# Kernel tuning notes

Measured on AMD Instinct MI355X. Metric: run time of the kernel, lower is better.

Reference implementation:

```python
import jax, jax.numpy as jnp
import numpy as np

CURV_BOUNDS = (-2.0, 2.0)
THRESH = 0.01   # |k| below this -> Euclidean branch
EPS = 1e-5

B, S, D = 4, 2048, 512


def setup_inputs() -> dict:
    key = jax.random.key(0)
    ks = jax.random.split(key, 8)
    x = jax.random.normal(ks[0], (B, S, D), jnp.float32)
    sc = 1.0 / np.sqrt(D)  # ~ nn.Linear default init scale
    Wq = jax.random.uniform(ks[1], (D, D), jnp.float32, -sc, sc)
    bq = jax.random.uniform(ks[2], (D,), jnp.float32, -sc, sc)
    Wk = jax.random.uniform(ks[3], (D, D), jnp.float32, -sc, sc)
    bk = jax.random.uniform(ks[4], (D,), jnp.float32, -sc, sc)
    Wv = jax.random.uniform(ks[5], (D, D), jnp.float32, -sc, sc)
    bv = jax.random.uniform(ks[6], (D,), jnp.float32, -sc, sc)
    curvature_raw = jnp.float32(0.5)   # init_curvature
    temperature = jnp.float32(1.0)
    mask = jnp.triu(jnp.ones((S, S), dtype=bool), 1)  # causal: True = masked out
    return {"x": x, "Wq": Wq, "bq": bq, "Wk": Wk, "bk": bk, "Wv": Wv,
            "bv": bv, "curvature_raw": curvature_raw,
            "temperature": temperature, "mask": mask}


def _curvature(raw):
    k_min, k_max = CURV_BOUNDS
    return k_min + (k_max - k_min) * (jnp.tanh(raw) + 1.0) / 2.0


def _project(u, k):
    # project_to_manifold: identity (euclid), Poincare-ball clip (k<0), sphere renorm (k>0)
    n = jnp.sqrt(jnp.sum(u * u, axis=-1, keepdims=True) + 1e-12)
    absk = jnp.abs(k)
    sk = jnp.sqrt(jnp.maximum(absk, EPS))
    max_norm = (1.0 - 1e-3) / sk                      # ball radius 1/sqrt(|k|)
    u_hyp = u * jnp.minimum(1.0, max_norm / n)
    u_sph = u / (n * sk)                              # sphere radius 1/sqrt(k)
    return jnp.where(absk < THRESH, u, jnp.where(k < 0, u_hyp, u_sph))


def reference(x, Wq, bq, Wk, bk, Wv, bv, curvature_raw, temperature, mask):
    k = _curvature(curvature_raw)
    q = x @ Wq.T + bq
    kk = x @ Wk.T + bk
    v = x @ Wv.T + bv
    qm = _project(q, k)
    km = _project(kk, k)

    # pairwise quantities without materializing [B,S,S,D]
    dots = jnp.einsum('bid,bjd->bij', qm, km)         # [B,S,S]
    qn2 = jnp.sum(qm * qm, axis=-1)                   # [B,S]
    kn2 = jnp.sum(km * km, axis=-1)                   # [B,S]
    diff2 = jnp.maximum(qn2[:, :, None] + kn2[:, None, :] - 2.0 * dots, 0.0)

    absk = jnp.abs(k)
    sk = jnp.sqrt(jnp.maximum(absk, EPS))

    d_euc = jnp.sqrt(diff2 + 1e-12)
    # hyperbolic (Poincare ball, c=|k|): acosh(1 + 2c|x-y|^2 / ((1-c|x|^2)(1-c|y|^2))) / sqrt(c)
    denom = jnp.maximum((1.0 - absk * qn2)[:, :, None] * (1.0 - absk * kn2)[:, None, :], EPS)
    arg = 1.0 + 2.0 * absk * diff2 / denom
    d_hyp = jnp.arccosh(jnp.maximum(arg, 1.0 + 1e-7)) / sk
    # spherical (radius 1/sqrt(k)): arccos(k * <x,y>) / sqrt(k)
    cosang = jnp.clip(absk * dots, -1.0 + 1e-7, 1.0 - 1e-7)
    d_sph = jnp.arccos(cosang) / sk

    dist = jnp.where(absk < THRESH, d_euc, jnp.where(k < 0, d_hyp, d_sph))

    scores = -dist / (temperature + 1e-8)
    scores = jnp.where(mask[None, :, :], -jnp.inf, scores)
    attention = jax.nn.softmax(scores, axis=-1)       # [B,S,S]
    output = jnp.einsum('bij,bjd->bid', attention, v) # [B,S,D]
    return output, attention
```

## Files before the change

### kernel.cpp

```cpp
#include <hip/hip_runtime.h>
#include <hip/hip_bf16.h>
#include <math.h>

typedef unsigned short u16;
typedef float float4e __attribute__((ext_vector_type(4)));
typedef short short8 __attribute__((ext_vector_type(8)));
typedef unsigned short ushort8 __attribute__((ext_vector_type(8)));
typedef unsigned short u16x4 __attribute__((ext_vector_type(4)));

#define SEQ 2048
#define DIM 512
#define NB  4

__device__ __forceinline__ float bf2f(u16 h) {
    return __uint_as_float(((unsigned)h) << 16);
}
__device__ __forceinline__ u16 f2bf(float f) {
    __hip_bfloat16 h = __float2bfloat16(f);
    return *reinterpret_cast<u16*>(&h);
}
__device__ __forceinline__ float curv_of(float raw) {
    return -2.0f + 2.0f * (tanhf(raw) + 1.0f);
}
__device__ __forceinline__ void gl_lds16(const u16* g, u16* lds) {
    __builtin_amdgcn_global_load_lds(
        (const __attribute__((address_space(1))) unsigned int*)g,
        (__attribute__((address_space(3))) unsigned int*)lds, 16, 0, 0);
}

__global__ __launch_bounds__(256) void cvt_all_kernel(
    const float* __restrict__ x, const float* __restrict__ Wq,
    const float* __restrict__ Wk, const float* __restrict__ Wv,
    u16* __restrict__ x_bf, u16* __restrict__ Wcat, float* __restrict__ lsum,
    float* __restrict__ outz)
{
    const int n_x = NB * SEQ * DIM, n_w = DIM * DIM;
    const int n_out = NB * SEQ * DIM;
    int gid = blockIdx.x * 256 + threadIdx.x;
    if (gid < NB * SEQ) lsum[gid] = 0.f;
    if (gid < n_out / 4) ((float4*)outz)[gid] = (float4){0.f, 0.f, 0.f, 0.f};
    int i4 = gid * 4;
    if (i4 < n_x) {
        float4 v = *(const float4*)&x[i4];
        u16x4 h = {f2bf(v.x), f2bf(v.y), f2bf(v.z), f2bf(v.w)};
        *(u16x4*)&x_bf[i4] = h;
    } else if (i4 < n_x + 3 * n_w) {
        int j = i4 - n_x;
        const float* W = (j < n_w) ? Wq : (j < 2 * n_w ? Wk : Wv);
        int off = j % n_w;
        float4 v = *(const float4*)&W[off];
        u16x4 h = {f2bf(v.x), f2bf(v.y), f2bf(v.z), f2bf(v.w)};
        *(u16x4*)&Wcat[j] = h;
    }
}

template<int MODE>
__global__ __launch_bounds__(256, 2) void gemm128_kernel(
    const u16* __restrict__ A, int lda, long long sA,
    const u16* __restrict__ Bt, int ldb, long long sB,
    void* __restrict__ Cv, int ldc, long long sC,
    u16* __restrict__ vT,
    float* __restrict__ lsum,
    const float* __restrict__ bq, const float* __restrict__ bk, const float* __restrict__ bv,
    const float* __restrict__ qn2v, const float* __restrict__ kn2v,
    const float* __restrict__ curvp, const float* __restrict__ tempp)
{
    int bn = blockIdx.x, bm = blockIdx.y, b = blockIdx.z;
    if (MODE == 1 && bn > bm) return;

    __shared__ __align__(16) u16 As[128 * 64];
    __shared__ __align__(16) u16 Bs[128 * 64];

    int t = threadIdx.x, wave = t >> 6, lane = t & 63;
    int wr = wave >> 1, wc = wave & 1;
    int lrow = lane & 15, quad = lane >> 4;
    int srow = lane >> 3, sc8 = lane & 7;

    const u16* Ab = A + (size_t)b * sA + (size_t)(bm * 128) * lda;
    const u16* Bb = Bt + (size_t)b * sB + (size_t)(bn * 128) * ldb;

    float4e acc[4][4];
#pragma unroll
    for (int i = 0; i < 4; i++)
#pragma unroll
        for (int j = 0; j < 4; j++) acc[i][j] = (float4e){0.f, 0.f, 0.f, 0.f};

    for (int kt = 0; kt < 8; ++kt) {
        int k0 = kt << 6;
        __syncthreads();
#pragma unroll
        for (int h = 0; h < 4; ++h) {
            int q = wave * 4 + h;
            int row = q * 8 + srow;
            int c = sc8 ^ (row & 7);
            gl_lds16(Ab + (size_t)row * lda + k0 + c * 8, &As[q * 512]);
            gl_lds16(Bb + (size_t)row * ldb + k0 + c * 8, &Bs[q * 512]);
        }
        __syncthreads();
#pragma unroll
        for (int kk = 0; kk < 2; ++kk) {
            short8 af[4], bfr[4];
#pragma unroll
            for (int im = 0; im < 4; im++) {
                int R = wr * 64 + im * 16 + lrow;
                af[im] = *(const short8*)&As[R * 64 + (((kk * 4 + quad) ^ (R & 7)) * 8)];
            }
#pragma unroll
            for (int in = 0; in < 4; in++) {
                int R = wc * 64 + in * 16 + lrow;
                bfr[in] = *(const short8*)&Bs[R * 64 + (((kk * 4 + quad) ^ (R & 7)) * 8)];
            }
#pragma unroll
            for (int im = 0; im < 4; im++)
#pragma unroll
                for (int in = 0; in < 4; in++)
                    acc[im][in] = __builtin_amdgcn_mfma_f32_16x16x32_bf16(af[im], bfr[in], acc[im][in], 0, 0, 0);
        }
    }

    if (MODE == 0) {
        u16* Cb = (u16*)Cv;
#pragma unroll
        for (int in = 0; in < 4; in++) {
            int gj = bn * 128 + wc * 64 + in * 16 + lrow;
            float bias = (gj < 512) ? bq[gj] : (gj < 1024 ? bk[gj - 512] : bv[gj - 1024]);
#pragma unroll
            for (int im = 0; im < 4; im++) {
                int gi0 = bm * 128 + wr * 64 + im * 16 + quad * 4;
                u16x4 pack;
#pragma unroll
                for (int r = 0; r < 4; r++) {
                    u16 hv = f2bf(acc[im][in][r] + bias);
                    Cb[(size_t)(gi0 + r) * ldc + gj] = hv;
                    pack[r] = hv;
                }
                if (gj >= 1024) {
                    int bb = gi0 >> 11, s = gi0 & 2047;
                    *(u16x4*)&vT[((size_t)bb * DIM + (gj - 1024)) * SEQ + s] = pack;
                }
            }
        }
    } else {
        float kv = curv_of(curvp[0]);
        float absk = fabsf(kv);
        float sk = sqrtf(fmaxf(absk, 1e-5f));
        float invT = 1.0f / (tempp[0] + 1e-8f);
        float Cexp = -1.4426950408889634f * invT;
        u16* Cb = (u16*)Cv + (size_t)b * sC;

        float psum[4][4];
#pragma unroll
        for (int im = 0; im < 4; im++)
#pragma unroll
            for (int r = 0; r < 4; r++) psum[im][r] = 0.f;

        float kn[4];
#pragma unroll
        for (int in = 0; in < 4; in++)
            kn[in] = kn2v[b * SEQ + bn * 128 + wc * 64 + in * 16 + lrow];

#pragma unroll
        for (int im = 0; im < 4; im++) {
#pragma unroll
            for (int r = 0; r < 4; r++) {
                int gi = bm * 128 + wr * 64 + im * 16 + quad * 4 + r;
                float qn = qn2v[b * SEQ + gi];
#pragma unroll
                for (int in = 0; in < 4; in++) {
                    int gj = bn * 128 + wc * 64 + in * 16 + lrow;
                    float dot = acc[im][in][r];
                    float diff2 = fmaxf(qn + kn[in] - 2.f * dot, 0.f);
                    float dist;
                    if (absk < 0.01f) {
                        dist = sqrtf(diff2 + 1e-12f);
                    } else if (kv < 0.f) {
                        float denom = fmaxf((1.f - absk * qn) * (1.f - absk * kn[in]), 1e-5f);
                        float arg = fmaxf(1.f + 2.f * absk * diff2 / denom, 1.f + 1e-7f);
                        dist = acoshf(arg) / sk;
                    } else {
                        float c = fminf(fmaxf(absk * dot, -1.f + 1e-7f), 1.f - 1e-7f);
                        dist = acosf(c) / sk;
                    }
                    float e = (gj <= gi) ? exp2f(dist * Cexp) : 0.f;
                    Cb[(size_t)gi * ldc + gj] = f2bf(e);
                    psum[im][r] += e;
                }
            }
        }
#pragma unroll
        for (int im = 0; im < 4; im++)
#pragma unroll
            for (int r = 0; r < 4; r++) {
                float v = psum[im][r];
                v += __shfl_xor(v, 1);
                v += __shfl_xor(v, 2);
                v += __shfl_xor(v, 4);
                v += __shfl_xor(v, 8);
                if (lrow == 0) {
                    int gi = bm * 128 + wr * 64 + im * 16 + quad * 4 + r;
                    atomicAdd(&lsum[b * SEQ + gi], v);
                }
            }
    }
}

template<int MODE>
__global__ __launch_bounds__(256, 8) void gemm64_kernel(
    const u16* __restrict__ A, int lda, long long sA,
    const u16* __restrict__ Bt, int ldb, long long sB,
    void* __restrict__ Cv, int ldc, long long sC,
    u16* __restrict__ vT,
    float* __restrict__ lsum,
    const float* __restrict__ bq, const float* __restrict__ bk, const float* __restrict__ bv,
    const float* __restrict__ qn2v, const float* __restrict__ kn2v,
    const float* __restrict__ curvp, const float* __restrict__ tempp)
{
    int bx = blockIdx.x, bm = blockIdx.y, b = blockIdx.z;
    int bn = (MODE == 2) ? (bx & 7) : bx;
    int kp = (MODE == 2) ? (bx >> 3) : 0;
    if (MODE == 1 && bn > bm) return;

    __shared__ __align__(16) u16 As[64 * 64];
    __shared__ __align__(16) u16 Bs[64 * 64];

    int t = threadIdx.x, wave = t >> 6, lane = t & 63;
    int wr = wave >> 1, wc = wave & 1;
    int lrow = lane & 15, quad = lane >> 4;
    int srow = lane >> 3, sc = lane & 7;

    const u16* Ab = A + (size_t)b * sA + (size_t)(bm * 64) * lda;
    const u16* Bb = Bt + (size_t)b * sB + (size_t)(bn * 64) * ldb;

    float4e acc[2][2];
#pragma unroll
    for (int i = 0; i < 2; i++)
#pragma unroll
        for (int j = 0; j < 2; j++) acc[i][j] = (float4e){0.f, 0.f, 0.f, 0.f};

    int ktBeg = (MODE == 2) ? kp : 0;
    int ktEnd = (MODE == 2) ? (bm + 1) : 8;
    int ktStp = (MODE == 2) ? 2 : 1;

    for (int kt = ktBeg; kt < ktEnd; kt += ktStp) {
        int k0 = kt << 6;
        __syncthreads();
#pragma unroll
        for (int h = 0; h < 2; ++h) {
            int q = wave * 2 + h;
            int row = q * 8 + srow;
            int c = sc ^ (row & 7);
            gl_lds16(Ab + (size_t)row * lda + k0 + c * 8, &As[q * 512]);
            gl_lds16(Bb + (size_t)row * ldb + k0 + c * 8, &Bs[q * 512]);
        }
        __syncthreads();
#pragma unroll
        for (int s = 0; s < 2; ++s) {
            short8 af[2], bfr[2];
#pragma unroll
            for (int im = 0; im < 2; im++) {
                int R = wr * 32 + im * 16 + lrow;
                af[im] = *(const short8*)&As[R * 64 + (((s * 4 + quad) ^ (R & 7)) * 8)];
            }
#pragma unroll
            for (int in = 0; in < 2; in++) {
                int R = wc * 32 + in * 16 + lrow;
                bfr[in] = *(const short8*)&Bs[R * 64 + (((s * 4 + quad) ^ (R & 7)) * 8)];
            }
#pragma unroll
            for (int im = 0; im < 2; im++)
#pragma unroll
                for (int in = 0; in < 2; in++)
                    acc[im][in] = __builtin_amdgcn_mfma_f32_16x16x32_bf16(af[im], bfr[in], acc[im][in], 0, 0, 0);
        }
    }

    if (MODE == 2) {
        float* Cb = (float*)Cv + (size_t)b * sC;
#pragma unroll
        for (int im = 0; im < 2; im++)
#pragma unroll
            for (int r = 0; r < 4; r++) {
                int gi = bm * 64 + wr * 32 + im * 16 + quad * 4 + r;
                float invl = 1.0f / lsum[b * SEQ + gi];
#pragma unroll
                for (int in = 0; in < 2; in++) {
                    int gd = bn * 64 + wc * 32 + in * 16 + lrow;
                    atomicAdd(&Cb[(size_t)gi * ldc + gd], acc[im][in][r] * invl);
                }
            }
    }
}

__global__ __launch_bounds__(256) void project_kernel(
    const u16* __restrict__ qkvh,
    u16* __restrict__ qm, u16* __restrict__ km,
    float* __restrict__ qn2, float* __restrict__ kn2,
    const float* __restrict__ curvp)
{
    int wave = threadIdx.x >> 6, lane = threadIdx.x & 63;
    int r = blockIdx.x * 4 + wave;
    float kv = curv_of(curvp[0]);
    float absk = fabsf(kv);
    float sk = sqrtf(fmaxf(absk, 1e-5f));

    const u16* qrow = qkvh + (size_t)r * 1536;
    ushort8 qh = *(const ushort8*)&qrow[lane * 8];
    ushort8 kh = *(const ushort8*)&qrow[512 + lane * 8];

    float qv[8], kw[8];
    float sq = 0.f, s2 = 0.f;
#pragma unroll
    for (int e = 0; e < 8; e++) {
        qv[e] = bf2f(qh[e]); sq += qv[e] * qv[e];
        kw[e] = bf2f(kh[e]); s2 += kw[e] * kw[e];
    }
#pragma unroll
    for (int off = 1; off < 64; off <<= 1) {
        sq += __shfl_xor(sq, off);
        s2 += __shfl_xor(s2, off);
    }

    float sclq, sclk;
    {
        float nq = sqrtf(sq + 1e-12f);
        float nk = sqrtf(s2 + 1e-12f);
        if (absk < 0.01f) { sclq = 1.f; sclk = 1.f; }
        else if (kv < 0.f) {
            float mx = (1.0f - 1e-3f) / sk;
            sclq = fminf(1.f, mx / nq);
            sclk = fminf(1.f, mx / nk);
        } else {
            sclq = 1.f / (nq * sk);
            sclk = 1.f / (nk * sk);
        }
    }
    if (lane == 0) {
        qn2[r] = sq * sclq * sclq;
        kn2[r] = s2 * sclk * sclk;
    }
    ushort8 qo, ko;
#pragma unroll
    for (int e = 0; e < 8; e++) {
        qo[e] = f2bf(qv[e] * sclq);
        ko[e] = f2bf(kw[e] * sclk);
    }
    *(ushort8*)&qm[(size_t)r * 512 + lane * 8] = qo;
    *(ushort8*)&km[(size_t)r * 512 + lane * 8] = ko;
}

__global__ __launch_bounds__(256) void norm_attn_kernel(
    const u16* __restrict__ attnH, const float* __restrict__ lsum,
    float* __restrict__ attnF)
{
    int i = blockIdx.x, b = blockIdx.y, t = threadIdx.x;
    float inv = 1.0f / lsum[b * SEQ + i];
    const u16* rowh = attnH + ((size_t)b * SEQ + i) * SEQ;
    float* row = attnF + ((size_t)b * SEQ + i) * SEQ;
    int L = i + 1;
    int j0 = t * 8;
    float4 lo, hi;
    if (j0 + 8 <= L) {
        ushort8 h = *(const ushort8*)&rowh[j0];
        lo.x = bf2f(h[0]) * inv; lo.y = bf2f(h[1]) * inv;
        lo.z = bf2f(h[2]) * inv; lo.w = bf2f(h[3]) * inv;
        hi.x = bf2f(h[4]) * inv; hi.y = bf2f(h[5]) * inv;
        hi.z = bf2f(h[6]) * inv; hi.w = bf2f(h[7]) * inv;
    } else {
        float v[8];
#pragma unroll
        for (int e = 0; e < 8; e++)
            v[e] = (j0 + e < L) ? bf2f(rowh[j0 + e]) * inv : 0.f;
        lo = (float4){v[0], v[1], v[2], v[3]};
        hi = (float4){v[4], v[5], v[6], v[7]};
    }
    *(float4*)&row[j0] = lo;
    *(float4*)&row[j0 + 4] = hi;
}

extern "C" void kernel_launch(void* const* d_in, const int* in_sizes, int n_in,
                              void* d_out, int out_size, void* d_ws, size_t ws_size,
                              hipStream_t stream) {
    (void)in_sizes; (void)n_in; (void)out_size; (void)ws_size;

    const float* x    = (const float*)d_in[0];
    const float* Wq   = (const float*)d_in[1];
    const float* bq   = (const float*)d_in[2];
    const float* Wk   = (const float*)d_in[3];
    const float* bk   = (const float*)d_in[4];
    const float* Wv   = (const float*)d_in[5];
    const float* bv   = (const float*)d_in[6];
    const float* curv = (const float*)d_in[7];
    const float* temp = (const float*)d_in[8];

    float* out   = (float*)d_out;
    float* attnF = out + (size_t)NB * SEQ * DIM;

    char* ws = (char*)d_ws;
    u16*   x_bf  = (u16*)(ws + 0);
    u16*   Wcat  = (u16*)(ws + 8388608);
    u16*   qkvh  = (u16*)(ws + 9961472);
    u16*   qm    = (u16*)(ws + 35127296);
    u16*   km    = (u16*)(ws + 43515904);
    u16*   vT    = (u16*)(ws + 51904512);
    float* qn2   = (float*)(ws + 60293120);
    float* kn2   = (float*)(ws + 60325888);
    float* lsum  = (float*)(ws + 60358656);
    u16*   attnH = (u16*)(ws + 0);

    {
        int n_tot = (NB * SEQ * DIM + 3 * DIM * DIM) / 4;
        cvt_all_kernel<<<(n_tot + 255) / 256, 256, 0, stream>>>(x, Wq, Wk, Wv, x_bf, Wcat, lsum, out);
    }

    gemm128_kernel<0><<<dim3(1536 / 128, 8192 / 128, 1), 256, 0, stream>>>(
        x_bf, 512, 0, Wcat, 512, 0, (void*)qkvh, 1536, 0,
        vT, nullptr, bq, bk, bv, nullptr, nullptr, nullptr, nullptr);

    project_kernel<<<NB * SEQ / 4, 256, 0, stream>>>(qkvh, qm, km, qn2, kn2, curv);

    gemm128_kernel<1><<<dim3(SEQ / 128, SEQ / 128, NB), 256, 0, stream>>>(
        qm, 512, (long long)SEQ * DIM, km, 512, (long long)SEQ * DIM,
        (void*)attnH, SEQ, (long long)SEQ * SEQ,
        nullptr, lsum, nullptr, nullptr, nullptr, qn2, kn2, curv, temp);

    gemm64_kernel<2><<<dim3(2 * DIM / 64, SEQ / 64, NB), 256, 0, stream>>>(
        attnH, SEQ, (long long)SEQ * SEQ, vT, SEQ, (long long)DIM * SEQ,
        (void*)out, DIM, (long long)SEQ * DIM,
        nullptr, lsum, nullptr, nullptr, nullptr, nullptr, nullptr, nullptr, nullptr);

    norm_attn_kernel<<<dim3(SEQ, NB), 256, 0, stream>>>(attnH, lsum, attnF);
}
```

Before: 247.7 us.

## Specialize GEMM kernels, drop split-K atomics in PV, use 128x64 score tiles

The templated GEMMs are split into dedicated QKV, score and PV kernels. The PV kernel no longer splits K across two blocks with atomicAdd into a zeroed output. It now loops over the full causal K range and writes its results directly, which also removes the output zeroing from the convert kernel. The score kernel moves from 128x128 to 128x64 tiles with occupancy 4, giving finer causal skipping and more blocks, in exchange for fewer PV blocks and more imbalance across rows.

```diff
diff --git a/kernel.cpp b/kernel.cpp
--- a/kernel.cpp
+++ b/kernel.cpp
@@ -31,14 +31,11 @@
 __global__ __launch_bounds__(256) void cvt_all_kernel(
     const float* __restrict__ x, const float* __restrict__ Wq,
     const float* __restrict__ Wk, const float* __restrict__ Wv,
-    u16* __restrict__ x_bf, u16* __restrict__ Wcat, float* __restrict__ lsum,
-    float* __restrict__ outz)
+    u16* __restrict__ x_bf, u16* __restrict__ Wcat, float* __restrict__ lsum)
 {
     const int n_x = NB * SEQ * DIM, n_w = DIM * DIM;
-    const int n_out = NB * SEQ * DIM;
     int gid = blockIdx.x * 256 + threadIdx.x;
     if (gid < NB * SEQ) lsum[gid] = 0.f;
-    if (gid < n_out / 4) ((float4*)outz)[gid] = (float4){0.f, 0.f, 0.f, 0.f};
     int i4 = gid * 4;
     if (i4 < n_x) {
         float4 v = *(const float4*)&x[i4];
@@ -54,19 +51,13 @@
     }
 }
 
-template<int MODE>
-__global__ __launch_bounds__(256, 2) void gemm128_kernel(
-    const u16* __restrict__ A, int lda, long long sA,
-    const u16* __restrict__ Bt, int ldb, long long sB,
-    void* __restrict__ Cv, int ldc, long long sC,
-    u16* __restrict__ vT,
-    float* __restrict__ lsum,
-    const float* __restrict__ bq, const float* __restrict__ bk, const float* __restrict__ bv,
-    const float* __restrict__ qn2v, const float* __restrict__ kn2v,
-    const float* __restrict__ curvp, const float* __restrict__ tempp)
-{
-    int bn = blockIdx.x, bm = blockIdx.y, b = blockIdx.z;
-    if (MODE == 1 && bn > bm) return;
+__global__ __launch_bounds__(256, 2) void gemm_qkv_kernel(
+    const u16* __restrict__ A, const u16* __restrict__ Bt,
+    u16* __restrict__ C, u16* __restrict__ vT,
+    const float* __restrict__ bq, const float* __restrict__ bk, const float* __restrict__ bv)
+{
+    const int lda = 512, ldb = 512, ldc = 1536;
+    int bn = blockIdx.x, bm = blockIdx.y;
 
     __shared__ __align__(16) u16 As[128 * 64];
     __shared__ __align__(16) u16 Bs[128 * 64];
@@ -76,8 +67,8 @@
     int lrow = lane & 15, quad = lane >> 4;
     int srow = lane >> 3, sc8 = lane & 7;
 
-    const u16* Ab = A + (size_t)b * sA + (size_t)(bm * 128) * lda;
-    const u16* Bb = Bt + (size_t)b * sB + (size_t)(bn * 128) * ldb;
+    const u16* Ab = A + (size_t)(bm * 128) * lda;
+    const u16* Bb = Bt + (size_t)(bn * 128) * ldb;
 
     float4e acc[4][4];
 #pragma unroll
@@ -118,107 +109,163 @@
         }
     }
 
-    if (MODE == 0) {
-        u16* Cb = (u16*)Cv;
-#pragma unroll
-        for (int in = 0; in < 4; in++) {
-            int gj = bn * 128 + wc * 64 + in * 16 + lrow;
-            float bias = (gj < 512) ? bq[gj] : (gj < 1024 ? bk[gj - 512] : bv[gj - 1024]);
-#pragma unroll
-            for (int im = 0; im < 4; im++) {
-                int gi0 = bm * 128 + wr * 64 + im * 16 + quad * 4;
-                u16x4 pack;
-#pragma unroll
-                for (int r = 0; r < 4; r++) {
-                    u16 hv = f2bf(acc[im][in][r] + bias);
-                    Cb[(size_t)(gi0 + r) * ldc + gj] = hv;
-                    pack[r] = hv;
-                }
-                if (gj >= 1024) {
-                    int bb = gi0 >> 11, s = gi0 & 2047;
-                    *(u16x4*)&vT[((size_t)bb * DIM + (gj - 1024)) * SEQ + s] = pack;
-                }
-            }
-        }
-    } else {
-        float kv = curv_of(curvp[0]);
-        float absk = fabsf(kv);
-        float sk = sqrtf(fmaxf(absk, 1e-5f));
-        float invT = 1.0f / (tempp[0] + 1e-8f);
-        float Cexp = -1.4426950408889634f * invT;
-        u16* Cb = (u16*)Cv + (size_t)b * sC;
-
-        float psum[4][4];
-#pragma unroll
-        for (int im = 0; im < 4; im++)
-#pragma unroll
-            for (int r = 0; r < 4; r++) psum[im][r] = 0.f;
-
-        float kn[4];
-#pragma unroll
-        for (int in = 0; in < 4; in++)
-            kn[in] = kn2v[b * SEQ + bn * 128 + wc * 64 + in * 16 + lrow];
-
+#pragma unroll
+    for (int in = 0; in < 4; in++) {
+        int gj = bn * 128 + wc * 64 + in * 16 + lrow;
+        float bias = (gj < 512) ? bq[gj] : (gj < 1024 ? bk[gj - 512] : bv[gj - 1024]);
 #pragma unroll
         for (int im = 0; im < 4; im++) {
+            int gi0 = bm * 128 + wr * 64 + im * 16 + quad * 4;
+            u16x4 pack;
 #pragma unroll
             for (int r = 0; r < 4; r++) {
-                int gi = bm * 128 + wr * 64 + im * 16 + quad * 4 + r;
-                float qn = qn2v[b * SEQ + gi];
-#pragma unroll
-                for (int in = 0; in < 4; in++) {
-                    int gj = bn * 128 + wc * 64 + in * 16 + lrow;
-                    float dot = acc[im][in][r];
-                    float diff2 = fmaxf(qn + kn[in] - 2.f * dot, 0.f);
-                    float dist;
-                    if (absk < 0.01f) {
-                        dist = sqrtf(diff2 + 1e-12f);
-                    } else if (kv < 0.f) {
-                        float denom = fmaxf((1.f - absk * qn) * (1.f - absk * kn[in]), 1e-5f);
-                        float arg = fmaxf(1.f + 2.f * absk * diff2 / denom, 1.f + 1e-7f);
-                        dist = acoshf(arg) / sk;
-                    } else {
-                        float c = fminf(fmaxf(absk * dot, -1.f + 1e-7f), 1.f - 1e-7f);
-                        dist = acosf(c) / sk;
-                    }
-                    float e = (gj <= gi) ? exp2f(dist * Cexp) : 0.f;
-                    Cb[(size_t)gi * ldc + gj] = f2bf(e);
-                    psum[im][r] += e;
-                }
-            }
-        }
-#pragma unroll
-        for (int im = 0; im < 4; im++)
-#pragma unroll
-            for (int r = 0; r < 4; r++) {
-                float v = psum[im][r];
-                v += __shfl_xor(v, 1);
-                v += __shfl_xor(v, 2);
-                v += __shfl_xor(v, 4);
-                v += __shfl_xor(v, 8);
-                if (lrow == 0) {
-                    int gi = bm * 128 + wr * 64 + im * 16 + quad * 4 + r;
-                    atomicAdd(&lsum[b * SEQ + gi], v);
-                }
-            }
-    }
-}
-
-template<int MODE>
-__global__ __launch_bounds__(256, 8) void gemm64_kernel(
-    const u16* __restrict__ A, int lda, long long sA,
-    const u16* __restrict__ Bt, int ldb, long long sB,
-    void* __restrict__ Cv, int ldc, long long sC,
-    u16* __restrict__ vT,
+                u16 hv = f2bf(acc[im][in][r] + bias);
+                C[(size_t)(gi0 + r) * ldc + gj] = hv;
+                pack[r] = hv;
+            }
+            if (gj >= 1024) {
+                int bb = gi0 >> 11, s = gi0 & 2047;
+                *(u16x4*)&vT[((size_t)bb * DIM + (gj - 1024)) * SEQ + s] = pack;
+            }
+        }
+    }
+}
+
+__global__ __launch_bounds__(256, 4) void gemm_scores_kernel(
+    const u16* __restrict__ qm, const u16* __restrict__ km,
+    u16* __restrict__ attnH,
     float* __restrict__ lsum,
-    const float* __restrict__ bq, const float* __restrict__ bk, const float* __restrict__ bv,
     const float* __restrict__ qn2v, const float* __restrict__ kn2v,
     const float* __restrict__ curvp, const float* __restrict__ tempp)
 {
-    int bx = blockIdx.x, bm = blockIdx.y, b = blockIdx.z;
-    int bn = (MODE == 2) ? (bx & 7) : bx;
-    int kp = (MODE == 2) ? (bx >> 3) : 0;
-    if (MODE == 1 && bn > bm) return;
+    const int lda = 512, ldb = 512, ldc = SEQ;
+    int bn = blockIdx.x, bm = blockIdx.y, b = blockIdx.z;
+    if (bn > 2 * bm + 1) return;
+
+    __shared__ __align__(16) u16 As[128 * 64];
+    __shared__ __align__(16) u16 Bs[64 * 64];
+
+    int t = threadIdx.x, wave = t >> 6, lane = t & 63;
+    int wr = wave >> 1, wc = wave & 1;
+    int lrow = lane & 15, quad = lane >> 4;
+    int srow = lane >> 3, sc8 = lane & 7;
+
+    const u16* Ab = qm + (size_t)b * SEQ * DIM + (size_t)(bm * 128) * lda;
+    const u16* Bb = km + (size_t)b * SEQ * DIM + (size_t)(bn * 64) * ldb;
+
+    float4e acc[4][2];
+#pragma unroll
+    for (int i = 0; i < 4; i++)
+#pragma unroll
+        for (int j = 0; j < 2; j++) acc[i][j] = (float4e){0.f, 0.f, 0.f, 0.f};
+
+    for (int kt = 0; kt < 8; ++kt) {
+        int k0 = kt << 6;
+        __syncthreads();
+#pragma unroll
+        for (int h = 0; h < 4; ++h) {
+            int q = wave * 4 + h;
+            int row = q * 8 + srow;
+            int c = sc8 ^ (row & 7);
+            gl_lds16(Ab + (size_t)row * lda + k0 + c * 8, &As[q * 512]);
+        }
+#pragma unroll
+        for (int h = 0; h < 2; ++h) {
+            int q = wave * 2 + h;
+            int row = q * 8 + srow;
+            int c = sc8 ^ (row & 7);
+            gl_lds16(Bb + (size_t)row * ldb + k0 + c * 8, &Bs[q * 512]);
+        }
+        __syncthreads();
+#pragma unroll
+        for (int kk = 0; kk < 2; ++kk) {
+            short8 af[4], bfr[2];
+#pragma unroll
+            for (int im = 0; im < 4; im++) {
+                int R = wr * 64 + im * 16 + lrow;
+                af[im] = *(const short8*)&As[R * 64 + (((kk * 4 + quad) ^ (R & 7)) * 8)];
+            }
+#pragma unroll
+            for (int in = 0; in < 2; in++) {
+                int R = wc * 32 + in * 16 + lrow;
+                bfr[in] = *(const short8*)&Bs[R * 64 + (((kk * 4 + quad) ^ (R & 7)) * 8)];
+            }
+#pragma unroll
+            for (int im = 0; im < 4; im++)
+#pragma unroll
+                for (int in = 0; in < 2; in++)
+                    acc[im][in] = __builtin_amdgcn_mfma_f32_16x16x32_bf16(af[im], bfr[in], acc[im][in], 0, 0, 0);
+        }
+    }
+
+    float kv = curv_of(curvp[0]);
+    float absk = fabsf(kv);
+    float sk = sqrtf(fmaxf(absk, 1e-5f));
+    float invT = 1.0f / (tempp[0] + 1e-8f);
+    float Cexp = -1.4426950408889634f * invT;
+    u16* Cb = attnH + (size_t)b * SEQ * SEQ;
+
+    float psum[4][4];
+#pragma unroll
+    for (int im = 0; im < 4; im++)
+#pragma unroll
+        for (int r = 0; r < 4; r++) psum[im][r] = 0.f;
+
+    float kn[2];
+#pragma unroll
+    for (int in = 0; in < 2; in++)
+        kn[in] = kn2v[b * SEQ + bn * 64 + wc * 32 + in * 16 + lrow];
+
+#pragma unroll
+    for (int im = 0; im < 4; im++) {
+#pragma unroll
+        for (int r = 0; r < 4; r++) {
+            int gi = bm * 128 + wr * 64 + im * 16 + quad * 4 + r;
+            float qn = qn2v[b * SEQ + gi];
+#pragma unroll
+            for (int in = 0; in < 2; in++) {
+                int gj = bn * 64 + wc * 32 + in * 16 + lrow;
+                float dot = acc[im][in][r];
+                float diff2 = fmaxf(qn + kn[in] - 2.f * dot, 0.f);
+                float dist;
+                if (absk < 0.01f) {
+                    dist = sqrtf(diff2 + 1e-12f);
+                } else if (kv < 0.f) {
+                    float denom = fmaxf((1.f - absk * qn) * (1.f - absk * kn[in]), 1e-5f);
+                    float arg = fmaxf(1.f + 2.f * absk * diff2 / denom, 1.f + 1e-7f);
+                    dist = acoshf(arg) / sk;
+                } else {
+                    float c = fminf(fmaxf(absk * dot, -1.f + 1e-7f), 1.f - 1e-7f);
+                    dist = acosf(c) / sk;
+                }
+                float e = (gj <= gi) ? exp2f(dist * Cexp) : 0.f;
+                Cb[(size_t)gi * ldc + gj] = f2bf(e);
+                psum[im][r] += e;
+            }
+        }
+    }
+#pragma unroll
+    for (int im = 0; im < 4; im++)
+#pragma unroll
+        for (int r = 0; r < 4; r++) {
+            float v = psum[im][r];
+            v += __shfl_xor(v, 1);
+            v += __shfl_xor(v, 2);
+            v += __shfl_xor(v, 4);
+            v += __shfl_xor(v, 8);
+            if (lrow == 0) {
+                int gi = bm * 128 + wr * 64 + im * 16 + quad * 4 + r;
+                atomicAdd(&lsum[b * SEQ + gi], v);
+            }
+        }
+}
+
+__global__ __launch_bounds__(256, 8) void gemm_pv_kernel(
+    const u16* __restrict__ attnH, const u16* __restrict__ vT,
+    float* __restrict__ out, const float* __restrict__ lsum)
+{
+    const int lda = SEQ, ldb = SEQ, ldc = DIM;
+    int bn = blockIdx.x, bm = blockIdx.y, b = blockIdx.z;
 
     __shared__ __align__(16) u16 As[64 * 64];
     __shared__ __align__(16) u16 Bs[64 * 64];
@@ -228,8 +275,8 @@
     int lrow = lane & 15, quad = lane >> 4;
     int srow = lane >> 3, sc = lane & 7;
 
-    const u16* Ab = A + (size_t)b * sA + (size_t)(bm * 64) * lda;
-    const u16* Bb = Bt + (size_t)b * sB + (size_t)(bn * 64) * ldb;
+    const u16* Ab = attnH + (size_t)b * SEQ * SEQ + (size_t)(bm * 64) * lda;
+    const u16* Bb = vT + (size_t)b * DIM * SEQ + (size_t)(bn * 64) * ldb;
 
     float4e acc[2][2];
 #pragma unroll
@@ -237,11 +284,7 @@
 #pragma unroll
         for (int j = 0; j < 2; j++) acc[i][j] = (float4e){0.f, 0.f, 0.f, 0.f};
 
-    int ktBeg = (MODE == 2) ? kp : 0;
-    int ktEnd = (MODE == 2) ? (bm + 1) : 8;
-    int ktStp = (MODE == 2) ? 2 : 1;
-
-    for (int kt = ktBeg; kt < ktEnd; kt += ktStp) {
+    for (int kt = 0; kt <= bm; ++kt) {
         int k0 = kt << 6;
         __syncthreads();
 #pragma unroll
@@ -274,21 +317,19 @@
         }
     }
 
-    if (MODE == 2) {
-        float* Cb = (float*)Cv + (size_t)b * sC;
-#pragma unroll
-        for (int im = 0; im < 2; im++)
-#pragma unroll
-            for (int r = 0; r < 4; r++) {
-                int gi = bm * 64 + wr * 32 + im * 16 + quad * 4 + r;
-                float invl = 1.0f / lsum[b * SEQ + gi];
-#pragma unroll
-                for (int in = 0; in < 2; in++) {
-                    int gd = bn * 64 + wc * 32 + in * 16 + lrow;
-                    atomicAdd(&Cb[(size_t)gi * ldc + gd], acc[im][in][r] * invl);
-                }
-            }
-    }
+    float* Cb = out + (size_t)b * SEQ * DIM;
+#pragma unroll
+    for (int im = 0; im < 2; im++)
+#pragma unroll
+        for (int r = 0; r < 4; r++) {
+            int gi = bm * 64 + wr * 32 + im * 16 + quad * 4 + r;
+            float invl = 1.0f / lsum[b * SEQ + gi];
+#pragma unroll
+            for (int in = 0; in < 2; in++) {
+                int gd = bn * 64 + wc * 32 + in * 16 + lrow;
+                Cb[(size_t)gi * ldc + gd] = acc[im][in][r] * invl;
+            }
+        }
 }
 
 __global__ __launch_bounds__(256) void project_kernel(
@@ -409,24 +450,19 @@
 
     {
         int n_tot = (NB * SEQ * DIM + 3 * DIM * DIM) / 4;
-        cvt_all_kernel<<<(n_tot + 255) / 256, 256, 0, stream>>>(x, Wq, Wk, Wv, x_bf, Wcat, lsum, out);
-    }
-
-    gemm128_kernel<0><<<dim3(1536 / 128, 8192 / 128, 1), 256, 0, stream>>>(
-        x_bf, 512, 0, Wcat, 512, 0, (void*)qkvh, 1536, 0,
-        vT, nullptr, bq, bk, bv, nullptr, nullptr, nullptr, nullptr);
+        cvt_all_kernel<<<(n_tot + 255) / 256, 256, 0, stream>>>(x, Wq, Wk, Wv, x_bf, Wcat, lsum);
+    }
+
+    gemm_qkv_kernel<<<dim3(1536 / 128, 8192 / 128, 1), 256, 0, stream>>>(
+        x_bf, Wcat, qkvh, vT, bq, bk, bv);
 
     project_kernel<<<NB * SEQ / 4, 256, 0, stream>>>(qkvh, qm, km, qn2, kn2, curv);
 
-    gemm128_kernel<1><<<dim3(SEQ / 128, SEQ / 128, NB), 256, 0, stream>>>(
-        qm, 512, (long long)SEQ * DIM, km, 512, (long long)SEQ * DIM,
-        (void*)attnH, SEQ, (long long)SEQ * SEQ,
-        nullptr, lsum, nullptr, nullptr, nullptr, qn2, kn2, curv, temp);
-
-    gemm64_kernel<2><<<dim3(2 * DIM / 64, SEQ / 64, NB), 256, 0, stream>>>(
-        attnH, SEQ, (long long)SEQ * SEQ, vT, SEQ, (long long)DIM * SEQ,
-        (void*)out, DIM, (long long)SEQ * DIM,
-        nullptr, lsum, nullptr, nullptr, nullptr, nullptr, nullptr, nullptr, nullptr);
+    gemm_scores_kernel<<<dim3(SEQ / 64, SEQ / 128, NB), 256, 0, stream>>>(
+        qm, km, attnH, lsum, qn2, kn2, curv, temp);
+
+    gemm_pv_kernel<<<dim3(DIM / 64, SEQ / 64, NB), 256, 0, stream>>>(
+        attnH, vT, out, lsum);
 
     norm_attn_kernel<<<dim3(SEQ, NB), 256, 0, stream>>>(attnH, lsum, attnF);
 }
```

Result: faster. 239.9 us (-3.1%).
